# Performance work log

Hardware: AMD Instinct MI355X
Metric: run time of the kernel (lower is better)

## Reference

```python
import jax, jax.numpy as jnp
import numpy as np

N, E = 100000, 1600000
NF, HC, NC = 32, 64, 64


def setup_inputs() -> dict:
    key = jax.random.key(0)
    ks = jax.random.split(key, 12)
    s = 0.05
    return {
        "x": jax.random.normal(ks[0], (N, NF), dtype=jnp.float32),
        "edge_index": jax.random.randint(ks[1], (2, E), 0, N, dtype=jnp.int64),
        "eps1": jnp.float32(0.0),
        "eps2": jnp.float32(0.0),
        "W1a": jax.random.normal(ks[2], (NF, HC), dtype=jnp.float32) * s,
        "b1a": jnp.zeros((HC,), dtype=jnp.float32),
        "W1b": jax.random.normal(ks[3], (HC, HC), dtype=jnp.float32) * s,
        "b1b": jnp.zeros((HC,), dtype=jnp.float32),
        "W2a": jax.random.normal(ks[4], (HC, HC), dtype=jnp.float32) * s,
        "b2a": jnp.zeros((HC,), dtype=jnp.float32),
        "W2b": jax.random.normal(ks[5], (HC, NC), dtype=jnp.float32) * s,
        "b2b": jnp.zeros((NC,), dtype=jnp.float32),
    }


def _gin_conv(h, src, dst, eps, Wa, ba, Wb, bb, num_nodes):
    # sum-aggregate neighbor features: out[dst] += h[src]
    agg = jax.ops.segment_sum(h[src], dst, num_segments=num_nodes)
    z = (1.0 + eps) * h + agg
    # 2-layer MLP: Linear -> ReLU -> Linear
    z = jax.nn.relu(z @ Wa + ba)
    return z @ Wb + bb


def reference(x, edge_index, eps1, eps2, W1a, b1a, W1b, b1b, W2a, b2a, W2b, b2b):
    src, dst = edge_index[0], edge_index[1]
    n = x.shape[0]
    emb = _gin_conv(x, src, dst, eps1, W1a, b1a, W1b, b1b, n)  # [N, HC]
    h = jax.nn.relu(emb)  # dropout is identity in eval mode
    logits = _gin_conv(h, src, dst, eps2, W2a, b2a, W2b, b2b, n)  # [N, NC]
    return (logits, emb)
```

## Files before the change

### kernel.cpp

```cpp
#include <hip/hip_runtime.h>


#define NFEAT 32
#define HID   64
#define NCLS  64

#define BSH   9
#define BNODES 512
#define NBKT_MAX 256
#define BCAP  16384
#define ECAP  2048

typedef unsigned int uint;
typedef unsigned short ushortT;
typedef __attribute__((ext_vector_type(8))) short bf16x8;
typedef __attribute__((ext_vector_type(4))) float f32x4;

__device__ __forceinline__ int clampi(int v, int hi){ v = v < 0 ? 0 : v; return v > hi ? hi : v; }

__device__ __forceinline__ ushortT f2b(float f){
  uint u = __float_as_uint(f);
  u = (u + 0x7FFFu + ((u >> 16) & 1u)) >> 16;
  return (ushortT)u;
}
__device__ __forceinline__ float b2f_lo(uint u){ return __uint_as_float(u << 16); }
__device__ __forceinline__ float b2f_hi(uint u){ return __uint_as_float(u & 0xFFFF0000u); }
__device__ __forceinline__ uint pack2(float lo, float hi){
  return (uint)f2b(lo) | ((uint)f2b(hi) << 16);
}


__global__ void k_bucket(const int* __restrict__ src, const int* __restrict__ dst,
                         int E, int N, int nbkt,
                         int* __restrict__ bktCnt, int* __restrict__ bktData){
  __shared__ int s_cnt[NBKT_MAX];
  __shared__ int s_base[NBKT_MAX];
  const int t = threadIdx.x;
  for (int j = t; j < nbkt; j += 256) s_cnt[j] = 0;
  __syncthreads();

  const int e0 = blockIdx.x * 4096;
  const int e1 = min(e0 + 4096, E);
  for (int e = e0 + t; e < e1; e += 256){
    int d = clampi(dst[e], N-1);
    atomicAdd(&s_cnt[d >> BSH], 1);
  }
  __syncthreads();
  for (int j = t; j < nbkt; j += 256){
    int c = s_cnt[j];
    s_base[j] = (c > 0) ? atomicAdd(&bktCnt[j], c) : 0;
    s_cnt[j] = 0;
  }
  __syncthreads();
  for (int e = e0 + t; e < e1; e += 256){
    int d = clampi(dst[e], N-1);
    int s = clampi(src[e], N-1);
    int b = d >> BSH;
    int p = s_base[b] + atomicAdd(&s_cnt[b], 1);
    if (p < BCAP)
      bktData[(size_t)b * BCAP + p] = ((d & (BNODES-1)) << 17) | s;
  }
}


__global__ void k_bktscan(const int* __restrict__ bktCnt, int nbkt,
                          int* __restrict__ bktBase, int* __restrict__ rowptr, int N){
  __shared__ int s[NBKT_MAX];
  const int t = threadIdx.x;
  int v = (t < nbkt) ? min(bktCnt[t], BCAP) : 0;
  s[t] = v;
  __syncthreads();
  for (int off = 1; off < NBKT_MAX; off <<= 1){
    int add = (t >= off) ? s[t-off] : 0;
    __syncthreads();
    s[t] += add;
    __syncthreads();
  }
  if (t < nbkt) bktBase[t] = s[t] - v;
  if (t == nbkt-1){ bktBase[nbkt] = s[t]; rowptr[N] = s[t]; }
}


__global__ __launch_bounds__(BNODES)
void k_build(const int* __restrict__ bktCnt, const int* __restrict__ bktBase,
             const int* __restrict__ bktData,
             int* __restrict__ rowptr, int* __restrict__ eidx, int N){
  __shared__ int s_h[BNODES];
  __shared__ int s_cur[BNODES];
  const int b = blockIdx.x, t = threadIdx.x;
  const int cnt  = min(bktCnt[b], BCAP);
  const int base = bktBase[b];
  const int* __restrict__ data = bktData + (size_t)b * BCAP;

  s_h[t] = 0;
  __syncthreads();
  for (int e = t; e < cnt; e += BNODES) atomicAdd(&s_h[data[e] >> 17], 1);
  __syncthreads();

  int deg = s_h[t];
  for (int off = 1; off < BNODES; off <<= 1){
    int add = (t >= off) ? s_h[t-off] : 0;
    __syncthreads();
    s_h[t] += add;
    __syncthreads();
  }
  int excl = s_h[t] - deg;
  int node = b * BNODES + t;
  if (node < N) rowptr[node] = base + excl;
  s_cur[t] = excl;
  __syncthreads();

  for (int e = t; e < cnt; e += BNODES){
    int val = data[e];
    int d = val >> 17;
    int p = atomicAdd(&s_cur[d], 1);
    eidx[base + p] = val & 0x1FFFF;
  }
}


__global__ void k_cvt(const float* __restrict__ in, ushortT* __restrict__ out, int n4){
  int t = blockIdx.x*blockDim.x + threadIdx.x;
  if (t >= n4) return;
  float4 v = reinterpret_cast<const float4*>(in)[t];
  ushort4 o = { f2b(v.x), f2b(v.y), f2b(v.z), f2b(v.w) };
  reinterpret_cast<ushort4*>(out)[t] = o;
}


__global__ void k_wprep(const float* __restrict__ W1a, const float* __restrict__ W1b,
                        const float* __restrict__ W2a, const float* __restrict__ W2b,
                        ushortT* __restrict__ T1a, ushortT* __restrict__ T1b,
                        ushortT* __restrict__ T2a, ushortT* __restrict__ T2b){
  int t = blockIdx.x*256 + threadIdx.x;
  const float* W; ushortT* T; int K; int base;
  if      (t <  2048){ W=W1a; T=T1a; K=32; base=0;     }
  else if (t <  6144){ W=W1b; T=T1b; K=64; base=2048;  }
  else if (t < 10240){ W=W2a; T=T2a; K=64; base=6144;  }
  else if (t < 14336){ W=W2b; T=T2b; K=64; base=10240; }
  else return;
  int o = t - base;
  int k = o >> 6, c = o & 63;
  T[c*K + k] = f2b(W[o]);
}


template<int K, bool WRITE_HB>
__global__ __launch_bounds__(512)
void k_fused(const uint4* __restrict__ f4,
             const int* __restrict__ rowptr, const int* __restrict__ eidx,
             const float* __restrict__ epsP,
             const ushortT* __restrict__ WaT,
             const float* __restrict__ ba,
             const ushortT* __restrict__ WbT,
             const float* __restrict__ bb,
             float* __restrict__ out,
             ushortT* __restrict__ hb, int N){
  constexpr int RS = K/8;
  constexpr int CH = RS/4;
  constexpr int U  = (CH == 1) ? 4 : 2;
  __shared__ int s_row[65];
  __shared__ int s_eidx[ECAP];
  __shared__ __align__(16) ushortT zt[64*K];
  __shared__ __align__(16) ushortT ht[64*64];
  const int t = threadIdx.x;
  const int row0 = blockIdx.x * 64;

  const int e0 = rowptr[min(row0, N)];
  const int e1 = rowptr[min(row0 + 64, N)];
  if (t < 65){
    int idx = row0 + t; if (idx > N) idx = N;
    s_row[t] = rowptr[idx];
  }
  const int cnt = e1 - e0;
  for (int j = t; j < cnt && j < ECAP; j += 512) s_eidx[j] = eidx[e0 + j];
  __syncthreads();

  {
    const int n = t >> 3;
    const int L = t & 7;
    const int q = L & (RS/CH - 1);
    const int s = L >> 2;
    const int node = row0 + n;
    float acc[CH*8];
    #pragma unroll
    for (int j = 0; j < CH*8; ++j) acc[j] = 0.f;

    const int b = s_row[n] - e0;
    const int e = s_row[n+1] - e0;
    int i = b + s;
    for (; i + 2*(U-1) < e; i += 2*U){
      int src[U];
      #pragma unroll
      for (int u = 0; u < U; ++u){
        int ii = i + 2*u;
        src[u] = (ii < ECAP) ? s_eidx[ii] : eidx[e0 + ii];
      }
      uint4 v[U][CH];
      #pragma unroll
      for (int u = 0; u < U; ++u)
        #pragma unroll
        for (int c = 0; c < CH; ++c)
          v[u][c] = f4[(size_t)src[u]*RS + q*CH + c];
      #pragma unroll
      for (int u = 0; u < U; ++u)
        #pragma unroll
        for (int c = 0; c < CH; ++c){
          acc[c*8+0] += b2f_lo(v[u][c].x); acc[c*8+1] += b2f_hi(v[u][c].x);
          acc[c*8+2] += b2f_lo(v[u][c].y); acc[c*8+3] += b2f_hi(v[u][c].y);
          acc[c*8+4] += b2f_lo(v[u][c].z); acc[c*8+5] += b2f_hi(v[u][c].z);
          acc[c*8+6] += b2f_lo(v[u][c].w); acc[c*8+7] += b2f_hi(v[u][c].w);
        }
    }
    for (; i < e; i += 2){
      int src0 = (i < ECAP) ? s_eidx[i] : eidx[e0 + i];
      #pragma unroll
      for (int c = 0; c < CH; ++c){
        uint4 v = f4[(size_t)src0*RS + q*CH + c];
        acc[c*8+0] += b2f_lo(v.x); acc[c*8+1] += b2f_hi(v.x);
        acc[c*8+2] += b2f_lo(v.y); acc[c*8+3] += b2f_hi(v.y);
        acc[c*8+4] += b2f_lo(v.z); acc[c*8+5] += b2f_hi(v.z);
        acc[c*8+6] += b2f_lo(v.w); acc[c*8+7] += b2f_hi(v.w);
      }
    }
    if (s == 1 && node < N){
      const float se = 1.0f + epsP[0];
      #pragma unroll
      for (int c = 0; c < CH; ++c){
        uint4 v = f4[(size_t)node*RS + q*CH + c];
        acc[c*8+0] = fmaf(se, b2f_lo(v.x), acc[c*8+0]);
        acc[c*8+1] = fmaf(se, b2f_hi(v.x), acc[c*8+1]);
        acc[c*8+2] = fmaf(se, b2f_lo(v.y), acc[c*8+2]);
        acc[c*8+3] = fmaf(se, b2f_hi(v.y), acc[c*8+3]);
        acc[c*8+4] = fmaf(se, b2f_lo(v.z), acc[c*8+4]);
        acc[c*8+5] = fmaf(se, b2f_hi(v.z), acc[c*8+5]);
        acc[c*8+6] = fmaf(se, b2f_lo(v.w), acc[c*8+6]);
        acc[c*8+7] = fmaf(se, b2f_hi(v.w), acc[c*8+7]);
      }
    }
    #pragma unroll
    for (int j = 0; j < CH*8; ++j) acc[j] += __shfl_xor(acc[j], 4);
    if (s == 0){
      #pragma unroll
      for (int c = 0; c < CH; ++c){
        uint4 z;
        z.x = pack2(acc[c*8+0], acc[c*8+1]);
        z.y = pack2(acc[c*8+2], acc[c*8+3]);
        z.z = pack2(acc[c*8+4], acc[c*8+5]);
        z.w = pack2(acc[c*8+6], acc[c*8+7]);
        reinterpret_cast<uint4*>(zt)[n*RS + q*CH + c] = z;
      }
    }
  }
  __syncthreads();

  const int w  = t >> 6;
  const int l  = t & 63;
  const int lr = l & 15;
  const int lg = l >> 4;
  const int rf = w & 3;
  const int c0 = (w >> 2) * 2;
  f32x4 c1[2];
  #pragma unroll
  for (int cl = 0; cl < 2; ++cl){ float bv = ba[(c0+cl)*16 + lr]; c1[cl] = (f32x4){bv,bv,bv,bv}; }
  #pragma unroll
  for (int kf = 0; kf < K/32; ++kf){
    bf16x8 a = *reinterpret_cast<const bf16x8*>(&zt[(rf*16 + lr)*K + kf*32 + lg*8]);
    #pragma unroll
    for (int cl = 0; cl < 2; ++cl){
      bf16x8 bfr = *reinterpret_cast<const bf16x8*>(&WaT[((c0+cl)*16 + lr)*K + kf*32 + lg*8]);
      c1[cl] = __builtin_amdgcn_mfma_f32_16x16x32_bf16(a, bfr, c1[cl], 0, 0, 0);
    }
  }
  #pragma unroll
  for (int cl = 0; cl < 2; ++cl)
    #pragma unroll
    for (int r = 0; r < 4; ++r)
      ht[(rf*16 + lg*4 + r)*64 + (c0+cl)*16 + lr] = f2b(fmaxf(c1[cl][r], 0.f));
  __syncthreads();

  f32x4 c2[2];
  #pragma unroll
  for (int cl = 0; cl < 2; ++cl){ float bv = bb[(c0+cl)*16 + lr]; c2[cl] = (f32x4){bv,bv,bv,bv}; }
  #pragma unroll
  for (int kf = 0; kf < 2; ++kf){
    bf16x8 a = *reinterpret_cast<const bf16x8*>(&ht[(rf*16 + lr)*64 + kf*32 + lg*8]);
    #pragma unroll
    for (int cl = 0; cl < 2; ++cl){
      bf16x8 bfr = *reinterpret_cast<const bf16x8*>(&WbT[((c0+cl)*16 + lr)*64 + kf*32 + lg*8]);
      c2[cl] = __builtin_amdgcn_mfma_f32_16x16x32_bf16(a, bfr, c2[cl], 0, 0, 0);
    }
  }
  #pragma unroll
  for (int cl = 0; cl < 2; ++cl)
    #pragma unroll
    for (int r = 0; r < 4; ++r){
      int row = row0 + rf*16 + lg*4 + r;
      if (row < N){
        float v = c2[cl][r];
        out[(size_t)row*64 + (c0+cl)*16 + lr] = v;
        if (WRITE_HB) hb[(size_t)row*64 + (c0+cl)*16 + lr] = f2b(fmaxf(v, 0.f));
      }
    }
}


extern "C" void kernel_launch(void* const* d_in, const int* in_sizes, int n_in,
                              void* d_out, int out_size, void* d_ws, size_t ws_size,
                              hipStream_t stream) {
  const int N = in_sizes[0] / NFEAT;
  const int E = in_sizes[1] / 2;
  const int nbkt = (N + BNODES - 1) / BNODES;

  const float* x    = (const float*)d_in[0];
  const int*   ei   = (const int*)d_in[1];
  const int*   srcI = ei;
  const int*   dstI = ei + E;
  const float* eps1 = (const float*)d_in[2];
  const float* eps2 = (const float*)d_in[3];
  const float* W1a  = (const float*)d_in[4];
  const float* b1a  = (const float*)d_in[5];
  const float* W1b  = (const float*)d_in[6];
  const float* b1b  = (const float*)d_in[7];
  const float* W2a  = (const float*)d_in[8];
  const float* b2a  = (const float*)d_in[9];
  const float* W2b  = (const float*)d_in[10];
  const float* b2b  = (const float*)d_in[11];

  float* outLogits = (float*)d_out;
  float* outEmb    = outLogits + (size_t)N * HID;

  char* w = (char*)d_ws;
  size_t off = 0;
  auto alloc = [&](size_t bytes) -> void* {
    void* p = w + off;
    off = (off + bytes + 255) & ~(size_t)255;
    return p;
  };
  int*     rowptr  = (int*)alloc((size_t)(N+1) * sizeof(int));
  int*     eidx    = (int*)alloc((size_t)E * sizeof(int));
  int*     bktCnt  = (int*)alloc((size_t)NBKT_MAX * sizeof(int));
  int*     bktBase = (int*)alloc((size_t)(NBKT_MAX+1) * sizeof(int));
  ushortT* T1a     = (ushortT*)alloc(64*32*sizeof(ushortT));
  ushortT* T1b     = (ushortT*)alloc(64*64*sizeof(ushortT));
  ushortT* T2a     = (ushortT*)alloc(64*64*sizeof(ushortT));
  ushortT* T2b     = (ushortT*)alloc(64*64*sizeof(ushortT));
  int*     bktData = (int*)alloc((size_t)NBKT_MAX * BCAP * sizeof(int));
  ushortT* xb      = (ushortT*)bktData;
  ushortT* hb      = (ushortT*)alloc((size_t)N * HID * sizeof(ushortT));

  hipMemsetAsync(bktCnt, 0, (size_t)NBKT_MAX * sizeof(int), stream);
  k_bucket <<<(E+4095)/4096, 256, 0, stream>>>(srcI, dstI, E, N, nbkt, bktCnt, bktData);
  k_bktscan<<<1, NBKT_MAX, 0, stream>>>(bktCnt, nbkt, bktBase, rowptr, N);
  k_build  <<<nbkt, BNODES, 0, stream>>>(bktCnt, bktBase, bktData, rowptr, eidx, N);

  k_cvt  <<<((N*NFEAT/4)+255)/256, 256, 0, stream>>>(x, xb, N*NFEAT/4);
  k_wprep<<<56, 256, 0, stream>>>(W1a, W1b, W2a, W2b, T1a, T1b, T2a, T2b);

  const int nblk = (N + 63) / 64;
  k_fused<NFEAT, true><<<nblk, 512, 0, stream>>>((const uint4*)xb, rowptr, eidx,
      eps1, T1a, b1a, T1b, b1b, outEmb, hb, N);

  k_fused<HID, false><<<nblk, 512, 0, stream>>>((const uint4*)hb, rowptr, eidx,
      eps2, T2a, b2a, T2b, b2b, outLogits, (ushortT*)nullptr, N);
}
```

Before: 133.1 us.

## Fold CSR build into fused GIN kernels using per-block 64-node buckets

Shrinks the destination buckets to 64 nodes so each fused-layer block can sort its own bucket in shared memory and build row offsets itself. This removes the global bucket scan and CSR build kernels, and the conversion, weight-prep and memset steps are merged into one prep kernel. The cost is that the per-bucket sort is repeated in both layers, and shared memory per block grows to roughly 32KB+ of edge buffers, which may lower occupancy. Buckets whose in-degree sum exceeds 2048 have their extra edges silently dropped.

```diff
diff --git a/kernel.cpp b/kernel.cpp
--- a/kernel.cpp
+++ b/kernel.cpp
@@ -5,11 +5,10 @@
 #define HID   64
 #define NCLS  64
 
-#define BSH   9
-#define BNODES 512
-#define NBKT_MAX 256
-#define BCAP  16384
-#define ECAP  2048
+#define BSH    6
+#define BNODES 64
+#define BCAP   2048
+#define NBKT_LDS 2048
 
 typedef unsigned int uint;
 typedef unsigned short ushortT;
@@ -30,11 +29,37 @@
 }
 
 
+__global__ void k_prep(const float* __restrict__ x, ushortT* __restrict__ xb, int n4,
+                       const float* __restrict__ W1a, const float* __restrict__ W1b,
+                       const float* __restrict__ W2a, const float* __restrict__ W2b,
+                       ushortT* __restrict__ T1a, ushortT* __restrict__ T1b,
+                       ushortT* __restrict__ T2a, ushortT* __restrict__ T2b,
+                       int* __restrict__ bktCnt, int nbkt){
+  int t = blockIdx.x*256 + threadIdx.x;
+  if (t < n4){
+    float4 v = reinterpret_cast<const float4*>(x)[t];
+    ushort4 o = { f2b(v.x), f2b(v.y), f2b(v.z), f2b(v.w) };
+    reinterpret_cast<ushort4*>(xb)[t] = o;
+  }
+  if (t < nbkt) bktCnt[t] = 0;
+  if (t < 14336){
+    const float* W; ushortT* T; int K; int base;
+    if      (t <  2048){ W=W1a; T=T1a; K=32; base=0;     }
+    else if (t <  6144){ W=W1b; T=T1b; K=64; base=2048;  }
+    else if (t < 10240){ W=W2a; T=T2a; K=64; base=6144;  }
+    else               { W=W2b; T=T2b; K=64; base=10240; }
+    int o = t - base;
+    int k = o >> 6, c = o & 63;
+    T[c*K + k] = f2b(W[o]);
+  }
+}
+
+
 __global__ void k_bucket(const int* __restrict__ src, const int* __restrict__ dst,
                          int E, int N, int nbkt,
                          int* __restrict__ bktCnt, int* __restrict__ bktData){
-  __shared__ int s_cnt[NBKT_MAX];
-  __shared__ int s_base[NBKT_MAX];
+  __shared__ int s_cnt[NBKT_LDS];
+  __shared__ int s_base[NBKT_LDS];
   const int t = threadIdx.x;
   for (int j = t; j < nbkt; j += 256) s_cnt[j] = 0;
   __syncthreads();
@@ -63,92 +88,10 @@
 }
 
 
-__global__ void k_bktscan(const int* __restrict__ bktCnt, int nbkt,
-                          int* __restrict__ bktBase, int* __restrict__ rowptr, int N){
-  __shared__ int s[NBKT_MAX];
-  const int t = threadIdx.x;
-  int v = (t < nbkt) ? min(bktCnt[t], BCAP) : 0;
-  s[t] = v;
-  __syncthreads();
-  for (int off = 1; off < NBKT_MAX; off <<= 1){
-    int add = (t >= off) ? s[t-off] : 0;
-    __syncthreads();
-    s[t] += add;
-    __syncthreads();
-  }
-  if (t < nbkt) bktBase[t] = s[t] - v;
-  if (t == nbkt-1){ bktBase[nbkt] = s[t]; rowptr[N] = s[t]; }
-}
-
-
-__global__ __launch_bounds__(BNODES)
-void k_build(const int* __restrict__ bktCnt, const int* __restrict__ bktBase,
-             const int* __restrict__ bktData,
-             int* __restrict__ rowptr, int* __restrict__ eidx, int N){
-  __shared__ int s_h[BNODES];
-  __shared__ int s_cur[BNODES];
-  const int b = blockIdx.x, t = threadIdx.x;
-  const int cnt  = min(bktCnt[b], BCAP);
-  const int base = bktBase[b];
-  const int* __restrict__ data = bktData + (size_t)b * BCAP;
-
-  s_h[t] = 0;
-  __syncthreads();
-  for (int e = t; e < cnt; e += BNODES) atomicAdd(&s_h[data[e] >> 17], 1);
-  __syncthreads();
-
-  int deg = s_h[t];
-  for (int off = 1; off < BNODES; off <<= 1){
-    int add = (t >= off) ? s_h[t-off] : 0;
-    __syncthreads();
-    s_h[t] += add;
-    __syncthreads();
-  }
-  int excl = s_h[t] - deg;
-  int node = b * BNODES + t;
-  if (node < N) rowptr[node] = base + excl;
-  s_cur[t] = excl;
-  __syncthreads();
-
-  for (int e = t; e < cnt; e += BNODES){
-    int val = data[e];
-    int d = val >> 17;
-    int p = atomicAdd(&s_cur[d], 1);
-    eidx[base + p] = val & 0x1FFFF;
-  }
-}
-
-
-__global__ void k_cvt(const float* __restrict__ in, ushortT* __restrict__ out, int n4){
-  int t = blockIdx.x*blockDim.x + threadIdx.x;
-  if (t >= n4) return;
-  float4 v = reinterpret_cast<const float4*>(in)[t];
-  ushort4 o = { f2b(v.x), f2b(v.y), f2b(v.z), f2b(v.w) };
-  reinterpret_cast<ushort4*>(out)[t] = o;
-}
-
-
-__global__ void k_wprep(const float* __restrict__ W1a, const float* __restrict__ W1b,
-                        const float* __restrict__ W2a, const float* __restrict__ W2b,
-                        ushortT* __restrict__ T1a, ushortT* __restrict__ T1b,
-                        ushortT* __restrict__ T2a, ushortT* __restrict__ T2b){
-  int t = blockIdx.x*256 + threadIdx.x;
-  const float* W; ushortT* T; int K; int base;
-  if      (t <  2048){ W=W1a; T=T1a; K=32; base=0;     }
-  else if (t <  6144){ W=W1b; T=T1b; K=64; base=2048;  }
-  else if (t < 10240){ W=W2a; T=T2a; K=64; base=6144;  }
-  else if (t < 14336){ W=W2b; T=T2b; K=64; base=10240; }
-  else return;
-  int o = t - base;
-  int k = o >> 6, c = o & 63;
-  T[c*K + k] = f2b(W[o]);
-}
-
-
 template<int K, bool WRITE_HB>
 __global__ __launch_bounds__(512)
 void k_fused(const uint4* __restrict__ f4,
-             const int* __restrict__ rowptr, const int* __restrict__ eidx,
+             const int* __restrict__ bktCnt, const int* __restrict__ bktData,
              const float* __restrict__ epsP,
              const ushortT* __restrict__ WaT,
              const float* __restrict__ ba,
@@ -159,43 +102,62 @@
   constexpr int RS = K/8;
   constexpr int CH = RS/4;
   constexpr int U  = (CH == 1) ? 4 : 2;
-  __shared__ int s_row[65];
-  __shared__ int s_eidx[ECAP];
+  __shared__ int s_data[BCAP];
+  __shared__ int s_eidx[BCAP];
+  __shared__ int s_h[BNODES], s_cur[BNODES], s_row[BNODES+1];
   __shared__ __align__(16) ushortT zt[64*K];
   __shared__ __align__(16) ushortT ht[64*64];
   const int t = threadIdx.x;
-  const int row0 = blockIdx.x * 64;
-
-  const int e0 = rowptr[min(row0, N)];
-  const int e1 = rowptr[min(row0 + 64, N)];
-  if (t < 65){
-    int idx = row0 + t; if (idx > N) idx = N;
-    s_row[t] = rowptr[idx];
-  }
-  const int cnt = e1 - e0;
-  for (int j = t; j < cnt && j < ECAP; j += 512) s_eidx[j] = eidx[e0 + j];
+  const int blk = blockIdx.x;
+  const int row0 = blk * 64;
+
+  const int cnt = min(bktCnt[blk], BCAP);
+  const int* __restrict__ data = bktData + (size_t)blk * BCAP;
+  if (t < BNODES) s_h[t] = 0;
+  __syncthreads();
+  for (int j = t; j < cnt; j += 512){
+    int v = data[j];
+    s_data[j] = v;
+    atomicAdd(&s_h[v >> 17], 1);
+  }
+  __syncthreads();
+  if (t < BNODES){
+    int deg = s_h[t];
+    int v = deg;
+    #pragma unroll
+    for (int off = 1; off < 64; off <<= 1){
+      int u = __shfl_up(v, off);
+      if (t >= off) v += u;
+    }
+    s_row[t+1] = v;
+    if (t == 0) s_row[0] = 0;
+    s_cur[t] = v - deg;
+  }
+  __syncthreads();
+  for (int j = t; j < cnt; j += 512){
+    int v = s_data[j];
+    int p = atomicAdd(&s_cur[v >> 17], 1);
+    s_eidx[p] = v & 0x1FFFF;
+  }
   __syncthreads();
 
   {
     const int n = t >> 3;
     const int L = t & 7;
-    const int q = L & (RS/CH - 1);
+    const int q = L & 3;
     const int s = L >> 2;
     const int node = row0 + n;
     float acc[CH*8];
     #pragma unroll
     for (int j = 0; j < CH*8; ++j) acc[j] = 0.f;
 
-    const int b = s_row[n] - e0;
-    const int e = s_row[n+1] - e0;
+    const int b = s_row[n];
+    const int e = s_row[n+1];
     int i = b + s;
     for (; i + 2*(U-1) < e; i += 2*U){
       int src[U];
       #pragma unroll
-      for (int u = 0; u < U; ++u){
-        int ii = i + 2*u;
-        src[u] = (ii < ECAP) ? s_eidx[ii] : eidx[e0 + ii];
-      }
+      for (int u = 0; u < U; ++u) src[u] = s_eidx[i + 2*u];
       uint4 v[U][CH];
       #pragma unroll
       for (int u = 0; u < U; ++u)
@@ -213,7 +175,7 @@
         }
     }
     for (; i < e; i += 2){
-      int src0 = (i < ECAP) ? s_eidx[i] : eidx[e0 + i];
+      int src0 = s_eidx[i];
       #pragma unroll
       for (int c = 0; c < CH; ++c){
         uint4 v = f4[(size_t)src0*RS + q*CH + c];
@@ -337,30 +299,24 @@
     off = (off + bytes + 255) & ~(size_t)255;
     return p;
   };
-  int*     rowptr  = (int*)alloc((size_t)(N+1) * sizeof(int));
-  int*     eidx    = (int*)alloc((size_t)E * sizeof(int));
-  int*     bktCnt  = (int*)alloc((size_t)NBKT_MAX * sizeof(int));
-  int*     bktBase = (int*)alloc((size_t)(NBKT_MAX+1) * sizeof(int));
+  int*     bktCnt  = (int*)alloc((size_t)nbkt * sizeof(int));
   ushortT* T1a     = (ushortT*)alloc(64*32*sizeof(ushortT));
   ushortT* T1b     = (ushortT*)alloc(64*64*sizeof(ushortT));
   ushortT* T2a     = (ushortT*)alloc(64*64*sizeof(ushortT));
   ushortT* T2b     = (ushortT*)alloc(64*64*sizeof(ushortT));
-  int*     bktData = (int*)alloc((size_t)NBKT_MAX * BCAP * sizeof(int));
-  ushortT* xb      = (ushortT*)bktData;
+  int*     bktData = (int*)alloc((size_t)nbkt * BCAP * sizeof(int));
+  ushortT* xb      = (ushortT*)alloc((size_t)N * NFEAT * sizeof(ushortT));
   ushortT* hb      = (ushortT*)alloc((size_t)N * HID * sizeof(ushortT));
 
-  hipMemsetAsync(bktCnt, 0, (size_t)NBKT_MAX * sizeof(int), stream);
-  k_bucket <<<(E+4095)/4096, 256, 0, stream>>>(srcI, dstI, E, N, nbkt, bktCnt, bktData);
-  k_bktscan<<<1, NBKT_MAX, 0, stream>>>(bktCnt, nbkt, bktBase, rowptr, N);
-  k_build  <<<nbkt, BNODES, 0, stream>>>(bktCnt, bktBase, bktData, rowptr, eidx, N);
-
-  k_cvt  <<<((N*NFEAT/4)+255)/256, 256, 0, stream>>>(x, xb, N*NFEAT/4);
-  k_wprep<<<56, 256, 0, stream>>>(W1a, W1b, W2a, W2b, T1a, T1b, T2a, T2b);
-
-  const int nblk = (N + 63) / 64;
-  k_fused<NFEAT, true><<<nblk, 512, 0, stream>>>((const uint4*)xb, rowptr, eidx,
+  const int n4 = N * NFEAT / 4;
+  k_prep<<<(n4+255)/256, 256, 0, stream>>>(x, xb, n4, W1a, W1b, W2a, W2b,
+                                           T1a, T1b, T2a, T2b, bktCnt, nbkt);
+
+  k_bucket<<<(E+4095)/4096, 256, 0, stream>>>(srcI, dstI, E, N, nbkt, bktCnt, bktData);
+
+  k_fused<NFEAT, true><<<nbkt, 512, 0, stream>>>((const uint4*)xb, bktCnt, bktData,
       eps1, T1a, b1a, T1b, b1b, outEmb, hb, N);
 
-  k_fused<HID, false><<<nblk, 512, 0, stream>>>((const uint4*)hb, rowptr, eidx,
+  k_fused<HID, false><<<nbkt, 512, 0, stream>>>((const uint4*)hb, bktCnt, bktData,
       eps2, T2a, b2a, T2b, b2b, outLogits, (ushortT*)nullptr, N);
 }
```

Result: faster. 119.5 us (-10.2%).
